# Kernel tuning notes

Hardware: AMD Instinct MI355X
Metric: run time of the kernel (lower is better)

Reference implementation:

```python
import jax, jax.numpy as jnp
import numpy as np
import math

B, N, K, C_IN, C_OUT = 2, 16384, 16, 128, 128


def _gather_neighbors(x, idx):
    # x: [B, N, C], idx: [B, N, K] -> [B, N, K, C]
    return jax.vmap(lambda xb, ib: xb[ib])(x, idx)


def setup_inputs() -> dict:
    key = jax.random.key(0)
    k1, k2, k3 = jax.random.split(key, 3)
    x = jax.random.normal(k1, (B, N, C_IN), dtype=jnp.float32)
    edge_index = jax.random.randint(k2, (2, B, N, K), 0, N, dtype=jnp.int64)
    W = jax.random.normal(k3, (C_OUT, C_IN), dtype=jnp.float32) * (1.0 / math.sqrt(C_IN))
    b = jnp.zeros((C_OUT,), dtype=jnp.float32)
    return {"x": x, "edge_index": edge_index, "W": W, "b": b}


def reference(x, edge_index, W, b):
    # x: [B, N, C]; edge_index: [2, B, N, K]
    x_i = _gather_neighbors(x, edge_index[1])  # [B, N, K, C] (centers)
    x_j = _gather_neighbors(x, edge_index[0])  # [B, N, K, C] (neighbors)
    scale = 1.0 / math.sqrt(x_i.shape[-1])
    scores = jnp.einsum('bnkc,bnjc->bnkj', x_i, x_j) * scale  # [B, N, K, K]
    p_attn = jax.nn.softmax(scores, axis=-1)
    h_k = jnp.einsum('bnkj,bnjc->bnkc', p_attn, x_j).sum(axis=-2)  # [B, N, C]
    y = (x + h_k) @ W.T + b  # Linear(in_channels -> out_channels)
    return jax.nn.relu(y)
```

## Files before the change

kernel.cpp:

```cpp
#include <hip/hip_runtime.h>
#include <hip/hip_bf16.h>
#include <math.h>

#define BB 2
#define NN 16384
#define KK 16
#define CC 128
#define COUT 128
#define NODES (BB * NN)
#define SP 136
#define SQP 136

typedef __attribute__((ext_vector_type(8))) short bf16x8;
typedef __attribute__((ext_vector_type(4))) float f32x4;
typedef __attribute__((ext_vector_type(2))) float f32x2;

__device__ __forceinline__ bf16x8 cvt8(f32x4 a, f32x4 b) {
    union { bf16x8 v; __hip_bfloat162 h[4]; } u;
    u.h[0] = __float22bfloat162_rn(make_float2(a[0], a[1]));
    u.h[1] = __float22bfloat162_rn(make_float2(a[2], a[3]));
    u.h[2] = __float22bfloat162_rn(make_float2(b[0], b[1]));
    u.h[3] = __float22bfloat162_rn(make_float2(b[2], b[3]));
    return u.v;
}

template <int CTRL>
__device__ __forceinline__ float rot_add(float v) {
    int r = __builtin_amdgcn_update_dpp(0, __float_as_int(v), CTRL, 0xF, 0xF, true);
    return v + __int_as_float(r);
}
__device__ __forceinline__ float row16_sum(float v) {
    v = rot_add<0x128>(v); v = rot_add<0x124>(v);
    v = rot_add<0x122>(v); v = rot_add<0x121>(v);
    return v;
}
__device__ __forceinline__ float row16_sum4(float v) {
    v = rot_add<0x128>(v); v = rot_add<0x124>(v);
    return v;
}

__global__ __launch_bounds__(256) void cast_x(
    const float* __restrict__ x,
    __hip_bfloat16* __restrict__ xh,
    unsigned char* __restrict__ xq)
{
    const int i = blockIdx.x * 256 + threadIdx.x;
    const f32x4* p = (const f32x4*)(x + (size_t)i * 8);
    f32x4 a = __builtin_nontemporal_load(p);
    f32x4 b = __builtin_nontemporal_load(p + 1);
    *(bf16x8*)(xh + (size_t)i * 8) = cvt8(a, b);
    int lo = __builtin_amdgcn_cvt_pk_fp8_f32(a[0], a[1], 0, false);
    lo     = __builtin_amdgcn_cvt_pk_fp8_f32(a[2], a[3], lo, true);
    int hi = __builtin_amdgcn_cvt_pk_fp8_f32(b[0], b[1], 0, false);
    hi     = __builtin_amdgcn_cvt_pk_fp8_f32(b[2], b[3], hi, true);
    int2 v; v.x = lo; v.y = hi;
    *(int2*)(xq + (size_t)i * 8) = v;
}

__device__ __forceinline__ float col_weight(f32x4 acc) {
    const float scale = 0.08838834764831843f;
    float w = 0.f;
    #pragma unroll
    for (int i = 0; i < 4; ++i) {
        float e = __expf(acc[i] * scale);
        float s = row16_sum(e);
        w += e * __builtin_amdgcn_rcpf(s);
    }
    w += __shfl_xor(w, 16, 64);
    w += __shfl_xor(w, 32, 64);
    return w;
}

__device__ __forceinline__ float2 reduce_h(const bf16x8* bfr, float wj,
                                           float* hb, int m, int q, int lane) {
    #pragma unroll
    for (int s = 0; s < 4; ++s) {
        union { bf16x8 v; unsigned short u[8]; } ub;
        ub.v = bfr[s];
        float f[8];
        #pragma unroll
        for (int e = 0; e < 8; ++e) {
            f[e] = __uint_as_float((unsigned)ub.u[e] << 16) * wj;
            f[e] = row16_sum4(f[e]);
        }
        if (m < 4) {
            f32x4 lo = {f[0], f[1], f[2], f[3]};
            f32x4 hi = {f[4], f[5], f[6], f[7]};
            *(f32x4*)&hb[m * 132 + 32 * s + 8 * q]     = lo;
            *(f32x4*)&hb[m * 132 + 32 * s + 8 * q + 4] = hi;
        }
    }
    float hx = 0.f, hy = 0.f;
    #pragma unroll
    for (int r = 0; r < 4; ++r) {
        float2 v = *(const float2*)&hb[r * 132 + 2 * lane];
        hx += v.x; hy += v.y;
    }
    return make_float2(hx, hy);
}

__global__ __launch_bounds__(256) void attn_phase(
    const __hip_bfloat16* __restrict__ xh,
    const unsigned char* __restrict__ xq,
    const int* __restrict__ edge,
    __hip_bfloat16* __restrict__ z)
{
    __shared__ __hip_bfloat16 stgj[4][16 * SP];
    __shared__ alignas(16) unsigned char stgq[4][16 * SQP];

    const int t = threadIdx.x;
    const int wv = t >> 6;
    const int lane = t & 63;
    const int m = lane & 15;
    const int q = lane >> 4;
    const int r = lane >> 4;
    const int c = lane & 15;

    const int node = blockIdx.x * 4 + wv;
    const int b = node >> 14;
    const __hip_bfloat16* xbh = xh + (size_t)b * (size_t)(NN * CC);
    const unsigned char*  xbq = xq + (size_t)b * (size_t)(NN * CC);
    __hip_bfloat16* sj = &stgj[wv][0];
    unsigned char*  sq = &stgq[wv][0];

    const int* ej = edge + (size_t)node * KK;
    const int* ei = ej + (size_t)NODES * KK;

    int2 ldq[4];
    #pragma unroll
    for (int g = 0; g < 4; ++g) {
        int ridx = __builtin_nontemporal_load(ei + g * 4 + r);
        ldq[g] = *(const int2*)(xbq + (size_t)ridx * CC + c * 8);
    }
    bf16x8 ldj[4];
    #pragma unroll
    for (int g = 0; g < 4; ++g) {
        int ridx = __builtin_nontemporal_load(ej + g * 4 + r);
        ldj[g] = *(const bf16x8*)(xbh + (size_t)ridx * CC + c * 8);
    }
    const int n0 = node & (NN - 1);
    __hip_bfloat162 rx = *(const __hip_bfloat162*)(xbh + (size_t)n0 * CC + 2 * lane);

    #pragma unroll
    for (int g = 0; g < 4; ++g)
        *(int2*)(sq + (g * 4 + r) * SQP + c * 8) = ldq[g];
    #pragma unroll
    for (int g = 0; g < 4; ++g)
        *(bf16x8*)(sj + (g * 4 + r) * SP + c * 8) = ldj[g];

    bf16x8 afr[4], bfr[4];
    #pragma unroll
    for (int s = 0; s < 4; ++s) {
        int2 wb = *(const int2*)(sq + m * SQP + s * 32 + q * 8);
        f32x2 f0 = __builtin_amdgcn_cvt_pk_f32_fp8(wb.x, false);
        f32x2 f1 = __builtin_amdgcn_cvt_pk_f32_fp8(wb.x, true);
        f32x2 f2 = __builtin_amdgcn_cvt_pk_f32_fp8(wb.y, false);
        f32x2 f3 = __builtin_amdgcn_cvt_pk_f32_fp8(wb.y, true);
        union { bf16x8 v; __hip_bfloat162 h[4]; } u;
        u.h[0] = __float22bfloat162_rn(make_float2(f0[0], f0[1]));
        u.h[1] = __float22bfloat162_rn(make_float2(f1[0], f1[1]));
        u.h[2] = __float22bfloat162_rn(make_float2(f2[0], f2[1]));
        u.h[3] = __float22bfloat162_rn(make_float2(f3[0], f3[1]));
        afr[s] = u.v;
        bfr[s] = *(const bf16x8*)(sj + m * SP + s * 32 + q * 8);
    }

    f32x4 acc = {0.f, 0.f, 0.f, 0.f};
    #pragma unroll
    for (int s = 0; s < 4; ++s)
        acc = __builtin_amdgcn_mfma_f32_16x16x32_bf16(afr[s], bfr[s], acc, 0, 0, 0);

    const float wj = col_weight(acc);

    float2 h = reduce_h(bfr, wj, (float*)sq, m, q, lane);

    float2 xc = __bfloat1622float2(rx);
    *(__hip_bfloat162*)(z + (size_t)node * CC + 2 * lane) =
        __float22bfloat162_rn(make_float2(xc.x + h.x, xc.y + h.y));
}

__global__ __launch_bounds__(256, 4) void linear_relu(
    const __hip_bfloat16* __restrict__ z,
    const float* __restrict__ W,
    const float* __restrict__ bias,
    float* __restrict__ out)
{
    const int t = threadIdx.x;
    const int lane = t & 63;
    const int wid = blockIdx.x * 4 + (t >> 6);
    const int ntile = wid & 7;
    const int m0 = wid >> 3;
    const int nm = lane & 15;
    const int nq = lane >> 4;

    const float* wp = W + (size_t)(ntile * 16 + nm) * CC + nq * 8;
    bf16x8 bfr[4];
    #pragma unroll
    for (int s = 0; s < 4; ++s) {
        f32x4 w0 = *(const f32x4*)(wp + 32 * s);
        f32x4 w1 = *(const f32x4*)(wp + 32 * s + 4);
        bfr[s] = cvt8(w0, w1);
    }
    const float bv = bias[ntile * 16 + nm];

    #pragma unroll
    for (int it = 0; it < 4; ++it) {
        const int mt = m0 + it * 512;
        const __hip_bfloat16* zp = z + (size_t)(mt * 16 + nm) * CC + nq * 8;
        bf16x8 afr[4];
        #pragma unroll
        for (int s = 0; s < 4; ++s)
            afr[s] = *(const bf16x8*)(zp + 32 * s);
        f32x4 acc = {0.f, 0.f, 0.f, 0.f};
        #pragma unroll
        for (int s = 0; s < 4; ++s)
            acc = __builtin_amdgcn_mfma_f32_16x16x32_bf16(afr[s], bfr[s], acc, 0, 0, 0);
        float* op = out + (size_t)(mt * 16 + nq * 4) * COUT + ntile * 16 + nm;
        #pragma unroll
        for (int i = 0; i < 4; ++i)
            op[(size_t)i * COUT] = fmaxf(acc[i] + bv, 0.f);
    }
}

extern "C" void kernel_launch(void* const* d_in, const int* in_sizes, int n_in,
                              void* d_out, int out_size, void* d_ws, size_t ws_size,
                              hipStream_t stream) {
    const float* x    = (const float*)d_in[0];
    const int*   edge = (const int*)d_in[1];
    const float* W    = (const float*)d_in[2];
    const float* bias = (const float*)d_in[3];
    float* out = (float*)d_out;
    __hip_bfloat16* z  = (__hip_bfloat16*)d_ws;
    __hip_bfloat16* xh = (__hip_bfloat16*)d_ws + (size_t)NODES * CC;
    unsigned char*  xq = (unsigned char*)d_ws + 16 * 1024 * 1024;

    cast_x<<<(NODES * CC) / (256 * 8), 256, 0, stream>>>(x, xh, xq);
    attn_phase<<<NODES / 4, 256, 0, stream>>>(xh, xq, edge, z);
    linear_relu<<<1024, 256, 0, stream>>>(z, W, bias, out);
}
```

Baseline: 113.2 us.

## Fuse attention aggregation with linear+ReLU and software-pipeline neighbor gathers

Merges the attention kernel and the linear/ReLU kernel so each block processes 16 nodes, keeps the z tile in shared memory and runs the 16x128x128 GEMM in the same block, removing the z round trip through global memory and one launch. Each wave now handles four nodes sequentially and prefetches the next node's neighbor gathers while computing the current one. W is pre-cast to bf16 by extra blocks in the cast kernel. The trade-off is more registers and shared memory per block, plus a block-wide sync and fewer blocks, which may reduce occupancy and latency hiding for the random gathers.

```diff
diff --git a/kernel.cpp b/kernel.cpp
--- a/kernel.cpp
+++ b/kernel.cpp
@@ -10,6 +10,8 @@
 #define NODES (BB * NN)
 #define SP 136
 #define SQP 136
+#define ZP 136
+#define XBLK 2048
 
 typedef __attribute__((ext_vector_type(8))) short bf16x8;
 typedef __attribute__((ext_vector_type(4))) float f32x4;
@@ -42,9 +44,20 @@
 __global__ __launch_bounds__(256) void cast_x(
     const float* __restrict__ x,
     __hip_bfloat16* __restrict__ xh,
-    unsigned char* __restrict__ xq)
+    unsigned char* __restrict__ xq,
+    const float* __restrict__ W,
+    __hip_bfloat16* __restrict__ wh)
 {
-    const int i = blockIdx.x * 256 + threadIdx.x;
+    const int bid = blockIdx.x;
+    if (bid >= XBLK) {
+        const int i = (bid - XBLK) * 256 + threadIdx.x;
+        const f32x4* p = (const f32x4*)(W + (size_t)i * 8);
+        f32x4 a = p[0];
+        f32x4 b = p[1];
+        *(bf16x8*)(wh + (size_t)i * 8) = cvt8(a, b);
+        return;
+    }
+    const int i = bid * 256 + threadIdx.x;
     const f32x4* p = (const f32x4*)(x + (size_t)i * 8);
     f32x4 a = __builtin_nontemporal_load(p);
     f32x4 b = __builtin_nontemporal_load(p + 1);
@@ -99,14 +112,46 @@
     return make_float2(hx, hy);
 }
 
-__global__ __launch_bounds__(256) void attn_phase(
+struct Gath { int2 q[4]; bf16x8 j[4]; __hip_bfloat162 rx; };
+
+__device__ __forceinline__ void gather_node(
+    int node, int r, int c, int lane,
     const __hip_bfloat16* __restrict__ xh,
     const unsigned char* __restrict__ xq,
     const int* __restrict__ edge,
-    __hip_bfloat16* __restrict__ z)
+    Gath& g)
+{
+    const int b = node >> 14;
+    const __hip_bfloat16* xbh = xh + (size_t)b * (size_t)(NN * CC);
+    const unsigned char*  xbq = xq + (size_t)b * (size_t)(NN * CC);
+    const int* ej = edge + (size_t)node * KK;
+    const int* ei = ej + (size_t)NODES * KK;
+    #pragma unroll
+    for (int gg = 0; gg < 4; ++gg) {
+        int ridx = __builtin_nontemporal_load(ei + gg * 4 + r);
+        g.q[gg] = *(const int2*)(xbq + (size_t)ridx * CC + c * 8);
+    }
+    #pragma unroll
+    for (int gg = 0; gg < 4; ++gg) {
+        int ridx = __builtin_nontemporal_load(ej + gg * 4 + r);
+        g.j[gg] = *(const bf16x8*)(xbh + (size_t)ridx * CC + c * 8);
+    }
+    const int n0 = node & (NN - 1);
+    g.rx = *(const __hip_bfloat162*)(xbh + (size_t)n0 * CC + 2 * lane);
+}
+
+__global__ __launch_bounds__(256, 4) void attn_fused(
+    const __hip_bfloat16* __restrict__ xh,
+    const unsigned char* __restrict__ xq,
+    const int* __restrict__ edge,
+    const __hip_bfloat16* __restrict__ wh,
+    const float* __restrict__ bias,
+    float* __restrict__ out)
 {
     __shared__ __hip_bfloat16 stgj[4][16 * SP];
     __shared__ alignas(16) unsigned char stgq[4][16 * SQP];
+    __shared__ alignas(16) float hbuf[4][544];
+    __shared__ __hip_bfloat16 zt[16][ZP];
 
     const int t = threadIdx.x;
     const int wv = t >> 6;
@@ -115,107 +160,80 @@
     const int q = lane >> 4;
     const int r = lane >> 4;
     const int c = lane & 15;
-
-    const int node = blockIdx.x * 4 + wv;
-    const int b = node >> 14;
-    const __hip_bfloat16* xbh = xh + (size_t)b * (size_t)(NN * CC);
-    const unsigned char*  xbq = xq + (size_t)b * (size_t)(NN * CC);
+    const int base = blockIdx.x * 16;
+
     __hip_bfloat16* sj = &stgj[wv][0];
     unsigned char*  sq = &stgq[wv][0];
 
-    const int* ej = edge + (size_t)node * KK;
-    const int* ei = ej + (size_t)NODES * KK;
-
-    int2 ldq[4];
-    #pragma unroll
-    for (int g = 0; g < 4; ++g) {
-        int ridx = __builtin_nontemporal_load(ei + g * 4 + r);
-        ldq[g] = *(const int2*)(xbq + (size_t)ridx * CC + c * 8);
-    }
-    bf16x8 ldj[4];
-    #pragma unroll
-    for (int g = 0; g < 4; ++g) {
-        int ridx = __builtin_nontemporal_load(ej + g * 4 + r);
-        ldj[g] = *(const bf16x8*)(xbh + (size_t)ridx * CC + c * 8);
-    }
-    const int n0 = node & (NN - 1);
-    __hip_bfloat162 rx = *(const __hip_bfloat162*)(xbh + (size_t)n0 * CC + 2 * lane);
-
-    #pragma unroll
-    for (int g = 0; g < 4; ++g)
-        *(int2*)(sq + (g * 4 + r) * SQP + c * 8) = ldq[g];
-    #pragma unroll
-    for (int g = 0; g < 4; ++g)
-        *(bf16x8*)(sj + (g * 4 + r) * SP + c * 8) = ldj[g];
-
-    bf16x8 afr[4], bfr[4];
-    #pragma unroll
-    for (int s = 0; s < 4; ++s) {
-        int2 wb = *(const int2*)(sq + m * SQP + s * 32 + q * 8);
-        f32x2 f0 = __builtin_amdgcn_cvt_pk_f32_fp8(wb.x, false);
-        f32x2 f1 = __builtin_amdgcn_cvt_pk_f32_fp8(wb.x, true);
-        f32x2 f2 = __builtin_amdgcn_cvt_pk_f32_fp8(wb.y, false);
-        f32x2 f3 = __builtin_amdgcn_cvt_pk_f32_fp8(wb.y, true);
-        union { bf16x8 v; __hip_bfloat162 h[4]; } u;
-        u.h[0] = __float22bfloat162_rn(make_float2(f0[0], f0[1]));
-        u.h[1] = __float22bfloat162_rn(make_float2(f1[0], f1[1]));
-        u.h[2] = __float22bfloat162_rn(make_float2(f2[0], f2[1]));
-        u.h[3] = __float22bfloat162_rn(make_float2(f3[0], f3[1]));
-        afr[s] = u.v;
-        bfr[s] = *(const bf16x8*)(sj + m * SP + s * 32 + q * 8);
-    }
-
-    f32x4 acc = {0.f, 0.f, 0.f, 0.f};
-    #pragma unroll
-    for (int s = 0; s < 4; ++s)
-        acc = __builtin_amdgcn_mfma_f32_16x16x32_bf16(afr[s], bfr[s], acc, 0, 0, 0);
-
-    const float wj = col_weight(acc);
-
-    float2 h = reduce_h(bfr, wj, (float*)sq, m, q, lane);
-
-    float2 xc = __bfloat1622float2(rx);
-    *(__hip_bfloat162*)(z + (size_t)node * CC + 2 * lane) =
-        __float22bfloat162_rn(make_float2(xc.x + h.x, xc.y + h.y));
-}
-
-__global__ __launch_bounds__(256, 4) void linear_relu(
-    const __hip_bfloat16* __restrict__ z,
-    const float* __restrict__ W,
-    const float* __restrict__ bias,
-    float* __restrict__ out)
-{
-    const int t = threadIdx.x;
-    const int lane = t & 63;
-    const int wid = blockIdx.x * 4 + (t >> 6);
-    const int ntile = wid & 7;
-    const int m0 = wid >> 3;
-    const int nm = lane & 15;
-    const int nq = lane >> 4;
-
-    const float* wp = W + (size_t)(ntile * 16 + nm) * CC + nq * 8;
-    bf16x8 bfr[4];
-    #pragma unroll
-    for (int s = 0; s < 4; ++s) {
-        f32x4 w0 = *(const f32x4*)(wp + 32 * s);
-        f32x4 w1 = *(const f32x4*)(wp + 32 * s + 4);
-        bfr[s] = cvt8(w0, w1);
-    }
-    const float bv = bias[ntile * 16 + nm];
+    Gath cur, nxt;
+    gather_node(base + wv * 4, r, c, lane, xh, xq, edge, cur);
 
     #pragma unroll
     for (int it = 0; it < 4; ++it) {
-        const int mt = m0 + it * 512;
-        const __hip_bfloat16* zp = z + (size_t)(mt * 16 + nm) * CC + nq * 8;
-        bf16x8 afr[4];
-        #pragma unroll
-        for (int s = 0; s < 4; ++s)
-            afr[s] = *(const bf16x8*)(zp + 32 * s);
+        #pragma unroll
+        for (int g = 0; g < 4; ++g)
+            *(int2*)(sq + (g * 4 + r) * SQP + c * 8) = cur.q[g];
+        #pragma unroll
+        for (int g = 0; g < 4; ++g)
+            *(bf16x8*)(sj + (g * 4 + r) * SP + c * 8) = cur.j[g];
+
+        if (it < 3)
+            gather_node(base + wv * 4 + it + 1, r, c, lane, xh, xq, edge, nxt);
+
+        bf16x8 afr[4], bfr[4];
+        #pragma unroll
+        for (int s = 0; s < 4; ++s) {
+            int2 wb = *(const int2*)(sq + m * SQP + s * 32 + q * 8);
+            f32x2 f0 = __builtin_amdgcn_cvt_pk_f32_fp8(wb.x, false);
+            f32x2 f1 = __builtin_amdgcn_cvt_pk_f32_fp8(wb.x, true);
+            f32x2 f2 = __builtin_amdgcn_cvt_pk_f32_fp8(wb.y, false);
+            f32x2 f3 = __builtin_amdgcn_cvt_pk_f32_fp8(wb.y, true);
+            union { bf16x8 v; __hip_bfloat162 h[4]; } u;
+            u.h[0] = __float22bfloat162_rn(make_float2(f0[0], f0[1]));
+            u.h[1] = __float22bfloat162_rn(make_float2(f1[0], f1[1]));
+            u.h[2] = __float22bfloat162_rn(make_float2(f2[0], f2[1]));
+            u.h[3] = __float22bfloat162_rn(make_float2(f3[0], f3[1]));
+            afr[s] = u.v;
+            bfr[s] = *(const bf16x8*)(sj + m * SP + s * 32 + q * 8);
+        }
+
         f32x4 acc = {0.f, 0.f, 0.f, 0.f};
         #pragma unroll
         for (int s = 0; s < 4; ++s)
             acc = __builtin_amdgcn_mfma_f32_16x16x32_bf16(afr[s], bfr[s], acc, 0, 0, 0);
-        float* op = out + (size_t)(mt * 16 + nq * 4) * COUT + ntile * 16 + nm;
+
+        const float wj = col_weight(acc);
+        float2 h = reduce_h(bfr, wj, &hbuf[wv][0], m, q, lane);
+
+        float2 xc = __bfloat1622float2(cur.rx);
+        const int row = wv * 4 + it;
+        *(__hip_bfloat162*)(&zt[row][2 * lane]) =
+            __float22bfloat162_rn(make_float2(xc.x + h.x, xc.y + h.y));
+
+        if (it < 3) cur = nxt;
+    }
+
+    __syncthreads();
+
+    bf16x8 zfr[4];
+    #pragma unroll
+    for (int s = 0; s < 4; ++s)
+        zfr[s] = *(const bf16x8*)(&zt[m][s * 32 + q * 8]);
+
+    #pragma unroll
+    for (int half = 0; half < 2; ++half) {
+        const int ct = wv * 2 + half;
+        const __hip_bfloat16* wp = wh + (size_t)(ct * 16 + m) * CC + q * 8;
+        bf16x8 wfr[4];
+        #pragma unroll
+        for (int s = 0; s < 4; ++s)
+            wfr[s] = *(const bf16x8*)(wp + s * 32);
+        const float bv = bias[ct * 16 + m];
+        f32x4 acc = {0.f, 0.f, 0.f, 0.f};
+        #pragma unroll
+        for (int s = 0; s < 4; ++s)
+            acc = __builtin_amdgcn_mfma_f32_16x16x32_bf16(zfr[s], wfr[s], acc, 0, 0, 0);
+        float* op = out + (size_t)(base + q * 4) * COUT + ct * 16 + m;
         #pragma unroll
         for (int i = 0; i < 4; ++i)
             op[(size_t)i * COUT] = fmaxf(acc[i] + bv, 0.f);
@@ -230,11 +248,10 @@
     const float* W    = (const float*)d_in[2];
     const float* bias = (const float*)d_in[3];
     float* out = (float*)d_out;
-    __hip_bfloat16* z  = (__hip_bfloat16*)d_ws;
-    __hip_bfloat16* xh = (__hip_bfloat16*)d_ws + (size_t)NODES * CC;
-    unsigned char*  xq = (unsigned char*)d_ws + 16 * 1024 * 1024;
-
-    cast_x<<<(NODES * CC) / (256 * 8), 256, 0, stream>>>(x, xh, xq);
-    attn_phase<<<NODES / 4, 256, 0, stream>>>(xh, xq, edge, z);
-    linear_relu<<<1024, 256, 0, stream>>>(z, W, bias, out);
-}
+    __hip_bfloat16* xh = (__hip_bfloat16*)d_ws;
+    unsigned char*  xq = (unsigned char*)d_ws + 8 * 1024 * 1024;
+    __hip_bfloat16* wh = (__hip_bfloat16*)((char*)d_ws + 12 * 1024 * 1024);
+
+    cast_x<<<XBLK + (COUT * CC) / (256 * 8), 256, 0, stream>>>(x, xh, xq, W, wh);
+    attn_fused<<<NODES / 16, 256, 0, stream>>>(xh, xq, edge, wh, bias, out);
+}
```

Result: faster. 107.7 us (-4.9%).
